# Kernel optimization log

Hardware: AMD Instinct MI355X
Metric: run time of the kernel (lower is better)

The kernel has to match this reference:

```python
import jax, jax.numpy as jnp
import numpy as np

P = 512   # pedestrians
E = 32    # embedding_dim
H = 64    # rela hidden dim


def setup_inputs() -> dict:
    key = jax.random.key(0)
    ks = jax.random.split(key, 8)
    return {
        "corr_index": jax.random.normal(ks[0], (P, P, 2), dtype=jnp.float32),
        "rela_ht": jax.random.normal(ks[1], (P, P, H), dtype=jnp.float32),
        "rela_ct": jax.random.normal(ks[2], (P, P, H), dtype=jnp.float32),
        "nei_index": jax.random.randint(ks[3], (P, P), 0, 2, dtype=jnp.int32),
        "W_emb": jax.random.normal(ks[4], (E, 2), dtype=jnp.float32) * 0.3,
        "b_emb": jnp.zeros((E,), dtype=jnp.float32),
        "W_ih": jax.random.normal(ks[5], (4 * H, E), dtype=jnp.float32) * 0.1,
        "W_hh": jax.random.normal(ks[6], (4 * H, H), dtype=jnp.float32) * 0.1,
        "b_ih": jnp.zeros((4 * H,), dtype=jnp.float32),
        "b_hh": jnp.zeros((4 * H,), dtype=jnp.float32),
    }


def reference(corr_index, rela_ht, rela_ct, nei_index, W_emb, b_emb, W_ih, W_hh, b_ih, b_hh):
    ped = corr_index.shape[0]
    hdim = rela_ht.shape[-1]
    # flatten pedestrian pairs: [P*P, ...]
    x = corr_index.reshape(ped * ped, 2)
    h = rela_ht.reshape(ped * ped, hdim)
    c = rela_ct.reshape(ped * ped, hdim)
    mask = (nei_index.reshape(-1) > 0)[:, None]  # [P*P, 1]

    # relative embedding + ReLU (dropout p=0 is identity)
    emb = jax.nn.relu(x @ W_emb.T + b_emb)  # [P*P, E]

    # torch LSTMCell math, gate order i, f, g, o
    gates = emb @ W_ih.T + b_ih + h @ W_hh.T + b_hh  # [P*P, 4H]
    i, f, g, o = jnp.split(gates, 4, axis=-1)
    i = jax.nn.sigmoid(i)
    f = jax.nn.sigmoid(f)
    g = jnp.tanh(g)
    o = jax.nn.sigmoid(o)
    c_new = f * c + i * g
    h_new = o * jnp.tanh(c_new)

    # scatter: only neighbor pairs (mask>0) are updated, others keep old state
    h_out = jnp.where(mask, h_new, h).reshape(ped, ped, hdim)
    c_out = jnp.where(mask, c_new, c).reshape(ped, ped, hdim)
    return h_out, c_out
```

## Files before the change

### kernel.cpp

```cpp
#include <hip/hip_runtime.h>
#include <hip/hip_bf16.h>

#define PED   512
#define HDIM  64
#define EDIM  32
#define NPAIR (PED * PED)
#define GATES 256
#define WF_ELEMS (16 * 64 * 24)
#define OS    68

typedef __attribute__((ext_vector_type(8))) __bf16 bf16x8;
typedef __attribute__((ext_vector_type(4))) float  floatx4;

__device__ __forceinline__ float sigmoidf_fast(float x) {
    return 1.0f / (1.0f + __expf(-x));
}
__device__ __forceinline__ float tanhf_fast(float x) {
    return 2.0f / (1.0f + __expf(-2.0f * x)) - 1.0f;
}

__global__ void sra_prep(const float* __restrict__ W_ih, const float* __restrict__ W_hh,
                         const float* __restrict__ b_ih, const float* __restrict__ b_hh,
                         __bf16* __restrict__ Wf, float* __restrict__ bsum)
{
    int tid = blockIdx.x * 256 + threadIdx.x;
    if (tid < WF_ELEMS) {
        int m    = tid % 24;
        int nl   = tid / 24;
        int lane = nl & 63;
        int nt   = nl >> 6;
        int n = nt * 16 + (lane & 15);
        int k = (m >> 3) * 32 + (lane >> 4) * 8 + (m & 7);
        float w = (k < EDIM) ? W_ih[n * EDIM + k] : W_hh[n * HDIM + (k - EDIM)];
        Wf[tid] = (__bf16)w;
    }
    if (tid < GATES) bsum[tid] = b_ih[tid] + b_hh[tid];
}

__global__ __launch_bounds__(256, 4)
void sra_main(const float* __restrict__ corr,
              const float* __restrict__ ht,
              const float* __restrict__ ct,
              const int*   __restrict__ nei,
              const float* __restrict__ W_emb,
              const float* __restrict__ b_emb,
              const __bf16* __restrict__ Wf,
              const float* __restrict__ bsumg,
              float* __restrict__ h_out,
              float* __restrict__ c_out)
{
    __shared__ float bsum[GATES];
    __shared__ __align__(16) float OhS[4][16 * OS];
    __shared__ __align__(16) float OcS[4][16 * OS];

    const int tid  = threadIdx.x;
    const int wave = tid >> 6;
    const int lane = tid & 63;
    const int lo   = lane & 15;
    const int qu   = lane >> 4;

    bsum[tid] = bsumg[tid];
    __syncthreads();

    float* oh = &OhS[wave][0];
    float* oc = &OcS[wave][0];

    const int tile = blockIdx.x * 4 + wave;
    const int rb   = tile * 16;

    float2 x = *(const float2*)(corr + (size_t)(rb + lo) * 2);
    bf16x8 a0;
#pragma unroll
    for (int j = 0; j < 8; ++j) {
        int e = qu * 8 + j;
        float v = fmaf(x.x, W_emb[e * 2 + 0], fmaf(x.y, W_emb[e * 2 + 1], b_emb[e]));
        a0[j] = (__bf16)fmaxf(v, 0.0f);
    }

    const size_t rowoff = (size_t)(rb + lo) * HDIM + qu * 8;
    float4 h0a = *(const float4*)(ht + rowoff);
    float4 h0b = *(const float4*)(ht + rowoff + 4);
    float4 h1a = *(const float4*)(ht + rowoff + 32);
    float4 h1b = *(const float4*)(ht + rowoff + 36);
    float4 c0a = *(const float4*)(ct + rowoff);
    float4 c0b = *(const float4*)(ct + rowoff + 4);
    float4 c1a = *(const float4*)(ct + rowoff + 32);
    float4 c1b = *(const float4*)(ct + rowoff + 36);

    float* ohr = oh + lo * OS + qu * 8;
    float* ocr = oc + lo * OS + qu * 8;
    *(float4*)(ohr)      = h0a;  *(float4*)(ohr + 4)  = h0b;
    *(float4*)(ohr + 32) = h1a;  *(float4*)(ohr + 36) = h1b;
    *(float4*)(ocr)      = c0a;  *(float4*)(ocr + 4)  = c0b;
    *(float4*)(ocr + 32) = c1a;  *(float4*)(ocr + 36) = c1b;

    bf16x8 a1, a2;
    a1[0] = (__bf16)h0a.x; a1[1] = (__bf16)h0a.y; a1[2] = (__bf16)h0a.z; a1[3] = (__bf16)h0a.w;
    a1[4] = (__bf16)h0b.x; a1[5] = (__bf16)h0b.y; a1[6] = (__bf16)h0b.z; a1[7] = (__bf16)h0b.w;
    a2[0] = (__bf16)h1a.x; a2[1] = (__bf16)h1a.y; a2[2] = (__bf16)h1a.z; a2[3] = (__bf16)h1a.w;
    a2[4] = (__bf16)h1b.x; a2[5] = (__bf16)h1b.y; a2[6] = (__bf16)h1b.z; a2[7] = (__bf16)h1b.w;

    floatx4 acc[16];
    const __bf16* bbase = Wf + lane * 24;
#pragma unroll
    for (int nt = 0; nt < 16; ++nt) {
        const __bf16* bp = bbase + nt * 1536;
        bf16x8 b0 = *(const bf16x8*)(bp);
        bf16x8 b1 = *(const bf16x8*)(bp + 8);
        bf16x8 b2 = *(const bf16x8*)(bp + 16);
        floatx4 c = {0.f, 0.f, 0.f, 0.f};
        c = __builtin_amdgcn_mfma_f32_16x16x32_bf16(a0, b0, c, 0, 0, 0);
        c = __builtin_amdgcn_mfma_f32_16x16x32_bf16(a1, b1, c, 0, 0, 0);
        c = __builtin_amdgcn_mfma_f32_16x16x32_bf16(a2, b2, c, 0, 0, 0);
        acc[nt] = c;
    }

    int msk[4];
#pragma unroll
    for (int r = 0; r < 4; ++r) msk[r] = nei[rb + qu * 4 + r];

#pragma unroll
    for (int tt = 0; tt < 4; ++tt) {
        const int k = tt * 16 + lo;
        const float bi  = bsum[k];
        const float bff = bsum[64 + k];
        const float bg  = bsum[128 + k];
        const float bo  = bsum[192 + k];
#pragma unroll
        for (int r = 0; r < 4; ++r) {
            const int rl = qu * 4 + r;
            float hold = oh[rl * OS + k];
            float cold = oc[rl * OS + k];
            float iv = sigmoidf_fast(acc[tt][r] + bi);
            float fv = sigmoidf_fast(acc[4 + tt][r] + bff);
            float gv = tanhf_fast(acc[8 + tt][r] + bg);
            float ov = sigmoidf_fast(acc[12 + tt][r] + bo);
            float cn = fv * cold + iv * gv;
            float hn = ov * tanhf_fast(cn);
            bool m = msk[r] > 0;
            oh[rl * OS + k] = m ? hn : hold;
            oc[rl * OS + k] = m ? cn : cold;
        }
    }

    float* hbase = h_out + (size_t)rb * HDIM;
    float* cbase = c_out + (size_t)rb * HDIM;
#pragma unroll
    for (int j = 0; j < 4; ++j) {
        int fi  = j * 64 + lane;
        int row = fi >> 4;
        int c4  = fi & 15;
        float4 vh = *(float4*)(oh + row * OS + c4 * 4);
        float4 vc = *(float4*)(oc + row * OS + c4 * 4);
        *(float4*)(hbase + fi * 4) = vh;
        *(float4*)(cbase + fi * 4) = vc;
    }
}

extern "C" void kernel_launch(void* const* d_in, const int* in_sizes, int n_in,
                              void* d_out, int out_size, void* d_ws, size_t ws_size,
                              hipStream_t stream) {
    const float* corr  = (const float*)d_in[0];
    const float* ht    = (const float*)d_in[1];
    const float* ct    = (const float*)d_in[2];
    const int*   nei   = (const int*)  d_in[3];
    const float* W_emb = (const float*)d_in[4];
    const float* b_emb = (const float*)d_in[5];
    const float* W_ih  = (const float*)d_in[6];
    const float* W_hh  = (const float*)d_in[7];
    const float* b_ih  = (const float*)d_in[8];
    const float* b_hh  = (const float*)d_in[9];

    __bf16* Wf   = (__bf16*)d_ws;
    float*  bsum = (float*)((char*)d_ws + WF_ELEMS * 2);

    float* hout = (float*)d_out;
    float* cout = hout + (size_t)NPAIR * HDIM;

    hipLaunchKernelGGL(sra_prep, dim3(96), dim3(256), 0, stream,
                       W_ih, W_hh, b_ih, b_hh, Wf, bsum);
    hipLaunchKernelGGL(sra_main, dim3(NPAIR / 64), dim3(256), 0, stream,
                       corr, ht, ct, nei, W_emb, b_emb, Wf, bsum, hout, cout);
}
```

Before: 310.5 us.

## Halve LDS staging, read old state directly from global, raise occupancy bound

Replaces the separate h and c shared-memory tiles with one reused tile. Old h/c values are now read straight from global memory in the epilogue, the new h is parked in the accumulator registers, and the h and c tiles are staged through LDS one after the other. The launch bound rises from 4 to 7 blocks per SM, and sigmoid/tanh use the hardware reciprocal instead of division. The aim is higher occupancy for this memory-bound kernel, at the cost of scattered, less coalesced global reads of old state (mostly L2 hits) and tighter register limits.

New measurement: 347.1 us. 11.8% more time.

```diff
diff --git a/kernel.cpp b/kernel.cpp
--- a/kernel.cpp
+++ b/kernel.cpp
@@ -13,10 +13,10 @@
 typedef __attribute__((ext_vector_type(4))) float  floatx4;
 
 __device__ __forceinline__ float sigmoidf_fast(float x) {
-    return 1.0f / (1.0f + __expf(-x));
+    return __builtin_amdgcn_rcpf(1.0f + __expf(-x));
 }
 __device__ __forceinline__ float tanhf_fast(float x) {
-    return 2.0f / (1.0f + __expf(-2.0f * x)) - 1.0f;
+    return fmaf(2.0f, __builtin_amdgcn_rcpf(1.0f + __expf(-2.0f * x)), -1.0f);
 }
 
 __global__ void sra_prep(const float* __restrict__ W_ih, const float* __restrict__ W_hh,
@@ -37,7 +37,7 @@
     if (tid < GATES) bsum[tid] = b_ih[tid] + b_hh[tid];
 }
 
-__global__ __launch_bounds__(256, 4)
+__global__ __launch_bounds__(256, 7)
 void sra_main(const float* __restrict__ corr,
               const float* __restrict__ ht,
               const float* __restrict__ ct,
@@ -50,8 +50,7 @@
               float* __restrict__ c_out)
 {
     __shared__ float bsum[GATES];
-    __shared__ __align__(16) float OhS[4][16 * OS];
-    __shared__ __align__(16) float OcS[4][16 * OS];
+    __shared__ __align__(16) float OT[4][16 * OS];
 
     const int tid  = threadIdx.x;
     const int wave = tid >> 6;
@@ -62,9 +61,7 @@
     bsum[tid] = bsumg[tid];
     __syncthreads();
 
-    float* oh = &OhS[wave][0];
-    float* oc = &OcS[wave][0];
-
+    float* ot = &OT[wave][0];
     const int tile = blockIdx.x * 4 + wave;
     const int rb   = tile * 16;
 
@@ -82,18 +79,6 @@
     float4 h0b = *(const float4*)(ht + rowoff + 4);
     float4 h1a = *(const float4*)(ht + rowoff + 32);
     float4 h1b = *(const float4*)(ht + rowoff + 36);
-    float4 c0a = *(const float4*)(ct + rowoff);
-    float4 c0b = *(const float4*)(ct + rowoff + 4);
-    float4 c1a = *(const float4*)(ct + rowoff + 32);
-    float4 c1b = *(const float4*)(ct + rowoff + 36);
-
-    float* ohr = oh + lo * OS + qu * 8;
-    float* ocr = oc + lo * OS + qu * 8;
-    *(float4*)(ohr)      = h0a;  *(float4*)(ohr + 4)  = h0b;
-    *(float4*)(ohr + 32) = h1a;  *(float4*)(ohr + 36) = h1b;
-    *(float4*)(ocr)      = c0a;  *(float4*)(ocr + 4)  = c0b;
-    *(float4*)(ocr + 32) = c1a;  *(float4*)(ocr + 36) = c1b;
-
     bf16x8 a1, a2;
     a1[0] = (__bf16)h0a.x; a1[1] = (__bf16)h0a.y; a1[2] = (__bf16)h0a.z; a1[3] = (__bf16)h0a.w;
     a1[4] = (__bf16)h0b.x; a1[5] = (__bf16)h0b.y; a1[6] = (__bf16)h0b.z; a1[7] = (__bf16)h0b.w;
@@ -119,6 +104,9 @@
 #pragma unroll
     for (int r = 0; r < 4; ++r) msk[r] = nei[rb + qu * 4 + r];
 
+    const float* ctb = ct + (size_t)rb * HDIM;
+    const float* htb = ht + (size_t)rb * HDIM;
+
 #pragma unroll
     for (int tt = 0; tt < 4; ++tt) {
         const int k = tt * 16 + lo;
@@ -129,8 +117,8 @@
 #pragma unroll
         for (int r = 0; r < 4; ++r) {
             const int rl = qu * 4 + r;
-            float hold = oh[rl * OS + k];
-            float cold = oc[rl * OS + k];
+            float cold = ctb[rl * HDIM + k];
+            float hold = htb[rl * HDIM + k];
             float iv = sigmoidf_fast(acc[tt][r] + bi);
             float fv = sigmoidf_fast(acc[4 + tt][r] + bff);
             float gv = tanhf_fast(acc[8 + tt][r] + bg);
@@ -138,8 +126,8 @@
             float cn = fv * cold + iv * gv;
             float hn = ov * tanhf_fast(cn);
             bool m = msk[r] > 0;
-            oh[rl * OS + k] = m ? hn : hold;
-            oc[rl * OS + k] = m ? cn : cold;
+            ot[rl * OS + k] = m ? cn : cold;
+            acc[tt][r]      = m ? hn : hold;
         }
     }
 
@@ -150,10 +138,24 @@
         int fi  = j * 64 + lane;
         int row = fi >> 4;
         int c4  = fi & 15;
-        float4 vh = *(float4*)(oh + row * OS + c4 * 4);
-        float4 vc = *(float4*)(oc + row * OS + c4 * 4);
+        float4 vc = *(float4*)(ot + row * OS + c4 * 4);
+        *(float4*)(cbase + fi * 4) = vc;
+    }
+
+#pragma unroll
+    for (int tt = 0; tt < 4; ++tt) {
+        const int k = tt * 16 + lo;
+#pragma unroll
+        for (int r = 0; r < 4; ++r)
+            ot[(qu * 4 + r) * OS + k] = acc[tt][r];
+    }
+#pragma unroll
+    for (int j = 0; j < 4; ++j) {
+        int fi  = j * 64 + lane;
+        int row = fi >> 4;
+        int c4  = fi & 15;
+        float4 vh = *(float4*)(ot + row * OS + c4 * 4);
         *(float4*)(hbase + fi * 4) = vh;
-        *(float4*)(cbase + fi * 4) = vc;
     }
 }
 
```
